# Kernel tuning notes

Measured on AMD Instinct MI355X. Metric: run time of the kernel, lower is better.

The kernel has to match this reference:

```python
import jax, jax.numpy as jnp
import numpy as np

WEIGHT = 1000000.0  # style loss weight


def gram_matrix(y):
    # y: [1, ch, h, w]. Original loops over channels i, taking a circular
    # window of local_ch=ch//2 channels and computing features @ features.T.
    # gram[i,a,b] = <F[(i+a)%ch], F[(i+b)%ch]> , so it is a modular gather of
    # the full ch x ch Gram matrix -- compute that once, then gather.
    b, ch, h, w = y.shape
    local_ch = ch // 2
    feats = y[0].reshape(ch, h * w)                      # [ch, hw]
    g_full = feats @ feats.T                             # [ch, ch]
    idx = (jnp.arange(ch)[:, None] + jnp.arange(local_ch)[None, :]) % ch  # [ch, lch]
    gram = g_full[idx[:, :, None], idx[:, None, :]]      # [ch, lch, lch]
    return gram / (b * local_ch * w * h)


def setup_inputs() -> dict:
    key = jax.random.key(0)
    k1, k2 = jax.random.split(key)
    x = jax.random.normal(k1, (1, 512, 64, 64), dtype=jnp.float32)
    target = jax.random.normal(k2, (512, 256, 256), dtype=jnp.float32)
    return {"x": x, "target": target}


def reference(x, target):
    # StyleLoss.forward with mode='loss', no mask: G = gram(x); loss = MSE(G, target)*weight.
    G = gram_matrix(x)
    loss = jnp.mean((G - target) ** 2) * WEIGHT
    return loss
```

## Files before the change

### kernel.cpp

```cpp
#include <hip/hip_runtime.h>
#include <hip/hip_bf16.h>


typedef __attribute__((ext_vector_type(8))) short bf16x8;
typedef __attribute__((ext_vector_type(4))) float f32x4;

#define CH 512
#define KDIM 4096
#define SPLITK 4

#define BM 64
#define BK 64
#define LDT 72

static __device__ inline uint4 cvt8_bf16(float4 a, float4 b) {
    float f[8] = {a.x, a.y, a.z, a.w, b.x, b.y, b.z, b.w};
    union { ushort u[8]; uint4 v; } o;
#pragma unroll
    for (int i = 0; i < 8; ++i) {
        __hip_bfloat16 h = __float2bfloat16(f[i]);
        o.u[i] = *reinterpret_cast<ushort*>(&h);
    }
    return o.v;
}

__global__ __launch_bounds__(256) void fused_main_kernel(const float* __restrict__ x,
                                                         const float* __restrict__ target,
                                                         float* __restrict__ g_part,
                                                         float* __restrict__ S1g,
                                                         float* __restrict__ t2part) {
    __shared__ __hip_bfloat16 a_tile[BM * LDT];
    __shared__ __hip_bfloat16 b_tile[BM * LDT];
    __shared__ float wavebuf[4][2][256];
    __shared__ float comb[4][512];
    __shared__ float t2w[4];

    const int bid = blockIdx.x;
    const int tid = threadIdx.x;
    const int lane = tid & 63;
    const int w    = tid >> 6;

    if (bid < 256) {
        const int bm = bid & 7, bn = (bid >> 3) & 7, kz = bid >> 6;
        const int m    = lane & 15;
        const int q    = lane >> 4;
        const int srow = tid >> 3;
        const int scol = (tid & 7) * 8;

        f32x4 acc[4] = {};

        const int NT = (KDIM / SPLITK) / BK;
        const int k0base = kz * (KDIM / SPLITK);

        const float* arow0 = x + (size_t)(bm * 64 + srow) * KDIM + k0base + scol;
        const float* brow0 = x + (size_t)(bn * 64 + srow) * KDIM + k0base + scol;

        float4 pa[2][2], pb[2][2];
#pragma unroll
        for (int p = 0; p < 2; ++p) {
            const float* ap = arow0 + (size_t)p * 32 * KDIM;
            const float* bp = brow0 + (size_t)p * 32 * KDIM;
            pa[p][0] = *(const float4*)(ap);  pa[p][1] = *(const float4*)(ap + 4);
            pb[p][0] = *(const float4*)(bp);  pb[p][1] = *(const float4*)(bp + 4);
        }

        for (int kt = 0; kt < NT; ++kt) {
            if (kt > 0) __syncthreads();
#pragma unroll
            for (int p = 0; p < 2; ++p) {
                uint4 av = cvt8_bf16(pa[p][0], pa[p][1]);
                uint4 bv = cvt8_bf16(pb[p][0], pb[p][1]);
                uint* ap = (uint*)(a_tile + (srow + p * 32) * LDT + scol);
                ap[0] = av.x; ap[1] = av.y; ap[2] = av.z; ap[3] = av.w;
                uint* bp = (uint*)(b_tile + (srow + p * 32) * LDT + scol);
                bp[0] = bv.x; bp[1] = bv.y; bp[2] = bv.z; bp[3] = bv.w;
            }
            __syncthreads();
            if (kt + 1 < NT) {
                const int ko = (kt + 1) * BK;
#pragma unroll
                for (int p = 0; p < 2; ++p) {
                    const float* ap = arow0 + (size_t)p * 32 * KDIM + ko;
                    const float* bp = brow0 + (size_t)p * 32 * KDIM + ko;
                    pa[p][0] = *(const float4*)(ap);  pa[p][1] = *(const float4*)(ap + 4);
                    pb[p][0] = *(const float4*)(bp);  pb[p][1] = *(const float4*)(bp + 4);
                }
            }
#pragma unroll
            for (int ks = 0; ks < 2; ++ks) {
                const int kk = ks * 32 + q * 8;
                bf16x8 afrag = *(const bf16x8*)(a_tile + (w * 16 + m) * LDT + kk);
#pragma unroll
                for (int j = 0; j < 4; ++j) {
                    bf16x8 bfrag = *(const bf16x8*)(b_tile + (j * 16 + m) * LDT + kk);
                    acc[j] = __builtin_amdgcn_mfma_f32_16x16x32_bf16(afrag, bfrag, acc[j], 0, 0, 0);
                }
            }
        }

        float* gp = g_part + ((size_t)kz << 18);
        const int col = lane & 15;
        const int rq  = (lane >> 4) * 4;
#pragma unroll
        for (int j = 0; j < 4; ++j) {
#pragma unroll
            for (int reg = 0; reg < 4; ++reg) {
                const int rg = bm * 64 + w * 16 + rq + reg;
                const int cg = bn * 64 + j * 16 + col;
                gp[rg * CH + cg] = acc[j][reg];
            }
        }
        return;
    }

    const int r = bid - 256;
    const float4* t4 = (const float4*)target;

    float accv[8] = {};
    float t2 = 0.0f;

    auto segload = [&](int s) -> float4 {
        const int a = w * 64 + s;
        const int i = (r - a) & 511;
        return t4[i * 16384 + a * 64 + lane];
    };
    auto process = [&](float4 v, int s, int p) {
        const int a = w * 64 + s;
        const int i = (r - a) & 511;
        t2 += v.x * v.x + v.y * v.y + v.z * v.z + v.w * v.w;
        *(float4*)&wavebuf[w][p][lane * 4] = v;
#pragma unroll
        for (int k = 0; k < 8; ++k) {
            const int b = (lane + 64 * k - i) & 511;
            if (b < 256) accv[k] += wavebuf[w][p][b];
        }
    };

    float4 va = segload(0), vb = segload(1);
    for (int s = 0; s < 64; s += 2) {
        float4 vn0 = {}, vn1 = {};
        if (s + 2 < 64) { vn0 = segload(s + 2); vn1 = segload(s + 3); }
        process(va, s, 0);
        process(vb, s + 1, 1);
        va = vn0; vb = vn1;
    }

#pragma unroll
    for (int k = 0; k < 8; ++k) comb[w][lane + 64 * k] = accv[k];
#pragma unroll
    for (int off = 32; off > 0; off >>= 1) t2 += __shfl_xor(t2, off, 64);
    if (lane == 0) t2w[w] = t2;
    __syncthreads();
    const float s0 = comb[0][tid]       + comb[1][tid]       + comb[2][tid]       + comb[3][tid];
    const float s1 = comb[0][tid + 256] + comb[1][tid + 256] + comb[2][tid + 256] + comb[3][tid + 256];
    S1g[r * CH + tid]       = s0;
    S1g[r * CH + tid + 256] = s1;
    if (tid == 0) t2part[r] = t2w[0] + t2w[1] + t2w[2] + t2w[3];
}

__global__ __launch_bounds__(256) void final_partial_kernel(const float* __restrict__ g_part,
                                                            const float* __restrict__ S1g,
                                                            float* __restrict__ partial2) {
    const float gscale = 1.0f / 1048576.0f;
    const int tid = threadIdx.x, bid = blockIdx.x;
    const int lane = tid & 63, wv = tid >> 6;
    const int cell = (bid * 256 + tid) * 4;
    const int r = cell >> 9, c0 = cell & 511;

    float4 g = *(const float4*)(g_part + cell);
#pragma unroll
    for (int sl = 1; sl < SPLITK; ++sl) {
        float4 v = *(const float4*)(g_part + sl * (CH * CH) + cell);
        g.x += v.x; g.y += v.y; g.z += v.z; g.w += v.w;
    }
    float4 s1 = *(const float4*)(S1g + cell);

    float gg[4] = {g.x, g.y, g.z, g.w};
    float ss[4] = {s1.x, s1.y, s1.z, s1.w};
    float acc = 0.0f;
#pragma unroll
    for (int j = 0; j < 4; ++j) {
        const int c  = c0 + j;
        const int d1 = (r - c) & 511;
        const int d2 = (c - r) & 511;
        const float n = (float)(256 - (d1 < d2 ? d1 : d2));
        const float gt = gg[j] * gscale;
        acc += n * gt * gt - 2.0f * gt * ss[j];
    }

#pragma unroll
    for (int off = 32; off > 0; off >>= 1) acc += __shfl_xor(acc, off, 64);
    __shared__ float wsum[4];
    if (lane == 0) wsum[wv] = acc;
    __syncthreads();
    if (tid == 0) partial2[bid] = wsum[0] + wsum[1] + wsum[2] + wsum[3];
}

__global__ __launch_bounds__(256) void finish_kernel(const float* __restrict__ partial2,
                                                     const float* __restrict__ t2part,
                                                     float* __restrict__ out) {
    const float lscale = 1.0e6f / 33554432.0f;
    const int tid  = threadIdx.x;
    const int lane = tid & 63;
    const int wv   = tid >> 6;
    float s = partial2[tid] + t2part[tid] + t2part[tid + 256];
#pragma unroll
    for (int off = 32; off > 0; off >>= 1) s += __shfl_xor(s, off, 64);
    __shared__ float wsum[4];
    if (lane == 0) wsum[wv] = s;
    __syncthreads();
    if (tid == 0) out[0] = (wsum[0] + wsum[1] + wsum[2] + wsum[3]) * lscale;
}

extern "C" void kernel_launch(void* const* d_in, const int* in_sizes, int n_in,
                              void* d_out, int out_size, void* d_ws, size_t ws_size,
                              hipStream_t stream) {
    const float* x      = (const float*)d_in[0];
    const float* target = (const float*)d_in[1];
    float* out = (float*)d_out;

    float* g_part   = (float*)d_ws;
    float* S1g      = g_part + SPLITK * CH * CH;
    float* t2part   = S1g + CH * CH;
    float* partial2 = t2part + CH;

    fused_main_kernel<<<768, 256, 0, stream>>>(x, target, g_part, S1g, t2part);
    final_partial_kernel<<<256, 256, 0, stream>>>(g_part, S1g, partial2);
    finish_kernel<<<1, 256, 0, stream>>>(partial2, t2part, out);
}
```

Baseline: 210.9 us.

## Read target with rotated gather instead of LDS scatter; reorder block roles

The target-reduction blocks no longer stage each 256-float segment through shared memory and then do masked scalar adds. Each lane now loads, directly from global memory, the four contiguous target values that map to its output columns after the modular shift, and accumulates them into two float4 halves selected by a mask. The GEMM blocks move to the end of the grid so the memory-bound target blocks dispatch first. The loads are rotated and unaligned, and wrapping segments take a scalar path, which may lower coalescing efficiency.

```diff
diff --git a/kernel.cpp b/kernel.cpp
--- a/kernel.cpp
+++ b/kernel.cpp
@@ -31,7 +31,6 @@
                                                          float* __restrict__ t2part) {
     __shared__ __hip_bfloat16 a_tile[BM * LDT];
     __shared__ __hip_bfloat16 b_tile[BM * LDT];
-    __shared__ float wavebuf[4][2][256];
     __shared__ float comb[4][512];
     __shared__ float t2w[4];
 
@@ -40,8 +39,9 @@
     const int lane = tid & 63;
     const int w    = tid >> 6;
 
-    if (bid < 256) {
-        const int bm = bid & 7, bn = (bid >> 3) & 7, kz = bid >> 6;
+    if (bid >= 512) {
+        const int gid = bid - 512;
+        const int bm = gid & 7, bn = (gid >> 3) & 7, kz = gid >> 6;
         const int m    = lane & 15;
         const int q    = lane >> 4;
         const int srow = tid >> 3;
@@ -113,40 +113,58 @@
         return;
     }
 
-    const int r = bid - 256;
-    const float4* t4 = (const float4*)target;
-
-    float accv[8] = {};
+    const int r = bid;
+
+    float4 acc0 = {0.f, 0.f, 0.f, 0.f};
+    float4 acc1 = {0.f, 0.f, 0.f, 0.f};
     float t2 = 0.0f;
 
-    auto segload = [&](int s) -> float4 {
+#pragma unroll 4
+    for (int s = 0; s < 64; ++s) {
         const int a = w * 64 + s;
         const int i = (r - a) & 511;
-        return t4[i * 16384 + a * 64 + lane];
-    };
-    auto process = [&](float4 v, int s, int p) {
-        const int a = w * 64 + s;
-        const int i = (r - a) & 511;
-        t2 += v.x * v.x + v.y * v.y + v.z * v.z + v.w * v.w;
-        *(float4*)&wavebuf[w][p][lane * 4] = v;
-#pragma unroll
-        for (int k = 0; k < 8; ++k) {
-            const int b = (lane + 64 * k - i) & 511;
-            if (b < 256) accv[k] += wavebuf[w][p][b];
-        }
-    };
-
-    float4 va = segload(0), vb = segload(1);
-    for (int s = 0; s < 64; s += 2) {
-        float4 vn0 = {}, vn1 = {};
-        if (s + 2 < 64) { vn0 = segload(s + 2); vn1 = segload(s + 3); }
-        process(va, s, 0);
-        process(vb, s + 1, 1);
-        va = vn0; vb = vn1;
-    }
-
-#pragma unroll
-    for (int k = 0; k < 8; ++k) comb[w][lane + 64 * k] = accv[k];
+        const int d = (4 * lane - i) & 511;
+        const int b = d & 255;
+        const int k0 = d >> 8;
+        const float* seg = target + ((size_t)i << 16) + (a << 8);
+
+        if (b <= 252) {
+            float4 t;
+            __builtin_memcpy(&t, seg + b, 16);
+            t2 += t.x * t.x + t.y * t.y + t.z * t.z + t.w * t.w;
+            const float m0 = k0 ? 0.0f : 1.0f;
+            const float m1 = 1.0f - m0;
+            acc0.x = __builtin_fmaf(t.x, m0, acc0.x);
+            acc0.y = __builtin_fmaf(t.y, m0, acc0.y);
+            acc0.z = __builtin_fmaf(t.z, m0, acc0.z);
+            acc0.w = __builtin_fmaf(t.w, m0, acc0.w);
+            acc1.x = __builtin_fmaf(t.x, m1, acc1.x);
+            acc1.y = __builtin_fmaf(t.y, m1, acc1.y);
+            acc1.z = __builtin_fmaf(t.z, m1, acc1.z);
+            acc1.w = __builtin_fmaf(t.w, m1, acc1.w);
+        } else {
+            const float mk0 = k0 ? 0.0f : 1.0f;
+            const float mw0 = 1.0f - mk0;
+            float v[4];
+            float m[4];
+            v[0] = seg[b];                 m[0] = mk0;
+            v[1] = seg[(b + 1) & 255];     m[1] = (b + 1 < 256) ? mk0 : mw0;
+            v[2] = seg[(b + 2) & 255];     m[2] = (b + 2 < 256) ? mk0 : mw0;
+            v[3] = seg[(b + 3) & 255];     m[3] = (b + 3 < 256) ? mk0 : mw0;
+            t2 += v[0] * v[0] + v[1] * v[1] + v[2] * v[2] + v[3] * v[3];
+            acc0.x = __builtin_fmaf(v[0], m[0], acc0.x);
+            acc0.y = __builtin_fmaf(v[1], m[1], acc0.y);
+            acc0.z = __builtin_fmaf(v[2], m[2], acc0.z);
+            acc0.w = __builtin_fmaf(v[3], m[3], acc0.w);
+            acc1.x = __builtin_fmaf(v[0], 1.0f - m[0], acc1.x);
+            acc1.y = __builtin_fmaf(v[1], 1.0f - m[1], acc1.y);
+            acc1.z = __builtin_fmaf(v[2], 1.0f - m[2], acc1.z);
+            acc1.w = __builtin_fmaf(v[3], 1.0f - m[3], acc1.w);
+        }
+    }
+
+    *(float4*)&comb[w][4 * lane]       = acc0;
+    *(float4*)&comb[w][4 * lane + 256] = acc1;
 #pragma unroll
     for (int off = 32; off > 0; off >>= 1) t2 += __shfl_xor(t2, off, 64);
     if (lane == 0) t2w[w] = t2;
```

After: 243.8 us. 1.16x slower.

## Reorder blocks so target reduction runs first, transpose LDS layout and deepen prefetch

Applied to the files above, without the earlier changes.

The fused kernel now gives blocks 0..511 to the target-streaming reduction and the last 256 blocks to the split-K Gram GEMM, so the heavier, bandwidth-bound work is dispatched first. The reduction stores each float4 segment in LDS as four strided planes and has each lane accumulate four contiguous output columns, split into two halves by select instead of a conditional. This replaces eight scattered conditional LDS reads with four computed-index reads, and the result is written back with float4 stores. Prefetch depth rises from two to four segments to keep more loads in flight, which costs more registers and makes the indexing harder to follow.

```diff
diff --git a/kernel.cpp b/kernel.cpp
--- a/kernel.cpp
+++ b/kernel.cpp
@@ -40,8 +40,9 @@
     const int lane = tid & 63;
     const int w    = tid >> 6;
 
-    if (bid < 256) {
-        const int bm = bid & 7, bn = (bid >> 3) & 7, kz = bid >> 6;
+    if (bid >= 512) {
+        const int gid = bid - 512;
+        const int bm = gid & 7, bn = (gid >> 3) & 7, kz = gid >> 6;
         const int m    = lane & 15;
         const int q    = lane >> 4;
         const int srow = tid >> 3;
@@ -113,48 +114,71 @@
         return;
     }
 
-    const int r = bid - 256;
-    const float4* t4 = (const float4*)target;
-
-    float accv[8] = {};
+    const int r = bid;
+    const float4* tgt4 = (const float4*)target;
+
+    float accA[4] = {}, accB[4] = {};
     float t2 = 0.0f;
-
-    auto segload = [&](int s) -> float4 {
-        const int a = w * 64 + s;
+    float* bufw = &wavebuf[w][0][0];
+
+    float4 pre[4];
+#pragma unroll
+    for (int e = 0; e < 4; ++e) {
+        const int a = 64 * w + e;
         const int i = (r - a) & 511;
-        return t4[i * 16384 + a * 64 + lane];
-    };
-    auto process = [&](float4 v, int s, int p) {
-        const int a = w * 64 + s;
-        const int i = (r - a) & 511;
-        t2 += v.x * v.x + v.y * v.y + v.z * v.z + v.w * v.w;
-        *(float4*)&wavebuf[w][p][lane * 4] = v;
-#pragma unroll
-        for (int k = 0; k < 8; ++k) {
-            const int b = (lane + 64 * k - i) & 511;
-            if (b < 256) accv[k] += wavebuf[w][p][b];
-        }
-    };
-
-    float4 va = segload(0), vb = segload(1);
-    for (int s = 0; s < 64; s += 2) {
-        float4 vn0 = {}, vn1 = {};
-        if (s + 2 < 64) { vn0 = segload(s + 2); vn1 = segload(s + 3); }
-        process(va, s, 0);
-        process(vb, s + 1, 1);
-        va = vn0; vb = vn1;
-    }
-
-#pragma unroll
-    for (int k = 0; k < 8; ++k) comb[w][lane + 64 * k] = accv[k];
+        pre[e] = tgt4[((size_t)i << 14) + (a << 6) + lane];
+    }
+
+    for (int s0 = 0; s0 < 64; s0 += 4) {
+        float4 cur[4];
+#pragma unroll
+        for (int e = 0; e < 4; ++e) cur[e] = pre[e];
+        if (s0 + 4 < 64) {
+#pragma unroll
+            for (int e = 0; e < 4; ++e) {
+                const int a = 64 * w + s0 + 4 + e;
+                const int i = (r - a) & 511;
+                pre[e] = tgt4[((size_t)i << 14) + (a << 6) + lane];
+            }
+        }
+#pragma unroll
+        for (int u = 0; u < 4; ++u) {
+            const int s = s0 + u;
+            const int a = 64 * w + s;
+            const int i = (r - a) & 511;
+            const float4 v = cur[u];
+            t2 += v.x * v.x + v.y * v.y + v.z * v.z + v.w * v.w;
+
+            float* buf = bufw + ((s & 1) << 8);
+            buf[lane]       = v.x;
+            buf[64 + lane]  = v.y;
+            buf[128 + lane] = v.z;
+            buf[192 + lane] = v.w;
+
+            const int b0  = (4 * lane - i) & 255;
+            const int k00 = ((4 * lane - i) & 511) >> 8;
+#pragma unroll
+            for (int e = 0; e < 4; ++e) {
+                const int pe   = b0 + e;
+                const int pos  = pe & 255;
+                const int k0   = k00 ^ (pe >> 8);
+                const float val = buf[(((e - i) & 3) << 6) | (pos >> 2)];
+                accA[e] += k0 ? 0.0f : val;
+                accB[e] += k0 ? val : 0.0f;
+            }
+        }
+    }
+
+    *(float4*)&comb[w][4 * lane]       = *(float4*)accA;
+    *(float4*)&comb[w][4 * lane + 256] = *(float4*)accB;
 #pragma unroll
     for (int off = 32; off > 0; off >>= 1) t2 += __shfl_xor(t2, off, 64);
     if (lane == 0) t2w[w] = t2;
     __syncthreads();
-    const float s0 = comb[0][tid]       + comb[1][tid]       + comb[2][tid]       + comb[3][tid];
-    const float s1 = comb[0][tid + 256] + comb[1][tid + 256] + comb[2][tid + 256] + comb[3][tid + 256];
-    S1g[r * CH + tid]       = s0;
-    S1g[r * CH + tid + 256] = s1;
+    const float s0c = comb[0][tid]       + comb[1][tid]       + comb[2][tid]       + comb[3][tid];
+    const float s1c = comb[0][tid + 256] + comb[1][tid + 256] + comb[2][tid + 256] + comb[3][tid + 256];
+    S1g[r * CH + tid]       = s0c;
+    S1g[r * CH + tid + 256] = s1c;
     if (tid == 0) t2part[r] = t2w[0] + t2w[1] + t2w[2] + t2w[3];
 }
 
```

Result: no change. 207.3 us (-1.7%).
